# Kernel tuning notes

Measured on AMD Instinct MI355X. Metric: run time of the kernel, lower is better.

## Reference

```python
import jax, jax.numpy as jnp
import numpy as np

B, N, F, D = 8, 2048, 128, 128


def setup_inputs() -> dict:
    key = jax.random.key(0)
    k1, k2, k3 = jax.random.split(key, 3)
    inputs = jax.random.normal(k1, (B, N, F), dtype=jnp.float32)
    adj = jax.random.uniform(k2, (B, N, N), dtype=jnp.float32)  # nonneg weights -> positive degrees
    W_kernel = jax.random.normal(k3, (F, D), dtype=jnp.float32) * (1.0 / np.sqrt(F))
    W_bias = jnp.zeros((D,), dtype=jnp.float32)
    return {"inputs": inputs, "adj": adj, "W_kernel": W_kernel, "W_bias": W_bias}


def _normalize_adjacency(adj):
    # D^{-1/2} A D^{-1/2}: same math as diag-matmul chain, via broadcast scaling
    d = jnp.sum(adj, axis=-1)                      # [B, N]
    d_sqrt_inv = jnp.power(d, -0.5)
    d_sqrt_inv = jnp.where(jnp.isinf(d_sqrt_inv), 0.0, d_sqrt_inv)
    return d_sqrt_inv[..., :, None] * adj * d_sqrt_inv[..., None, :]


def reference(inputs, adj, W_kernel, W_bias):
    adj_norm = _normalize_adjacency(adj)           # [B, N, N]
    feats = inputs @ W_kernel + W_bias             # [B, N, D]
    out = jnp.einsum('bnm,bmd->bnd', adj_norm, feats)
    return jax.nn.relu(out)
```

## Files before the change

### kernel.cpp

```cpp
#include <hip/hip_runtime.h>
#include <hip/hip_bf16.h>
#include <stdint.h>

#define B_ 8
#define N_ 2048
#define F_ 128
#define D_ 128

typedef short bf16x8 __attribute__((ext_vector_type(8)));
typedef float f32x4 __attribute__((ext_vector_type(4)));

__device__ __forceinline__ unsigned short f2bf(float f) {
    unsigned u = __float_as_uint(f);
    u += 0x7fffu + ((u >> 16) & 1u);
    return (unsigned short)(u >> 16);
}

__global__ __launch_bounds__(256) void k_degwt(const float* __restrict__ adj,
                                               const float* __restrict__ W,
                                               float* __restrict__ rs,
                                               unsigned short* __restrict__ Wt) {
    if (blockIdx.x < 4096) {
        const int wave = threadIdx.x >> 6, lane = threadIdx.x & 63;
        const int row = blockIdx.x * 4 + wave;
        const float4* p = (const float4*)(adj + (size_t)row * N_);
        float s = 0.f;
#pragma unroll
        for (int j = 0; j < 8; ++j) {
            float4 v = p[j * 64 + lane];
            s += (v.x + v.y) + (v.z + v.w);
        }
#pragma unroll
        for (int m = 1; m < 64; m <<= 1) s += __shfl_xor(s, m, 64);
        if (lane == 0) rs[row] = (s > 0.f) ? (1.0f / sqrtf(s)) : 0.f;
    } else {
        int c = (blockIdx.x - 4096) * 256 + threadIdx.x;
        int d = c >> 4, f0 = (c & 15) * 8;
        union { bf16x8 v; unsigned short u[8]; } pk;
#pragma unroll
        for (int e = 0; e < 8; ++e) pk.u[e] = f2bf(W[(size_t)(f0 + e) * D_ + d]);
        *(bf16x8*)(Wt + (size_t)d * F_ + f0) = pk.v;
    }
}

__global__ __launch_bounds__(256) void k_feat(const float* __restrict__ x,
                                              const unsigned short* __restrict__ Wt,
                                              const float* __restrict__ bias,
                                              const float* __restrict__ rs,
                                              unsigned short* __restrict__ gt) {
    __shared__ __align__(16) unsigned char sX[64 * 128 * 2];
    __shared__ __align__(16) unsigned char sW[128 * 128 * 2];
    const int t = threadIdx.x;
    const int R0 = blockIdx.x * 64;

#pragma unroll
    for (int j = 0; j < 8; ++j) {
        int c = j * 256 + t;
        unsigned L = (unsigned)c * 16u;
        unsigned lg = L ^ (((L >> 8) & 7u) << 4);
        const unsigned char* src = (const unsigned char*)Wt + lg;
        __builtin_amdgcn_global_load_lds(
            (const __attribute__((address_space(1))) void*)src,
            (__attribute__((address_space(3))) void*)(sW + L), 16, 0, 0);
    }
#pragma unroll
    for (int j = 0; j < 4; ++j) {
        int c = j * 256 + t;
        int row = c >> 4, sub = c & 15;
        const float4* src = (const float4*)(x + (size_t)(R0 + row) * F_ + sub * 8);
        float4 v0 = src[0], v1 = src[1];
        union { bf16x8 v; unsigned short u[8]; } pk;
        pk.u[0] = f2bf(v0.x); pk.u[1] = f2bf(v0.y); pk.u[2] = f2bf(v0.z); pk.u[3] = f2bf(v0.w);
        pk.u[4] = f2bf(v1.x); pk.u[5] = f2bf(v1.y); pk.u[6] = f2bf(v1.z); pk.u[7] = f2bf(v1.w);
        unsigned byte = (unsigned)(row * 256 + sub * 16);
        byte ^= ((byte >> 8) & 7u) << 4;
        *(bf16x8*)(sX + byte) = pk.v;
    }
    __syncthreads();

    const int w = t >> 6, l = t & 63, lr = l & 15, lh = l >> 4;
    f32x4 acc[8];
#pragma unroll
    for (int j = 0; j < 8; ++j) acc[j] = (f32x4){0.f, 0.f, 0.f, 0.f};

#pragma unroll
    for (int ks = 0; ks < 4; ++ks) {
        unsigned abyte = (unsigned)((w * 16 + lr) * 256 + lh * 16 + ks * 64);
        abyte ^= ((abyte >> 8) & 7u) << 4;
        bf16x8 a = *(const bf16x8*)(sX + abyte);
#pragma unroll
        for (int j = 0; j < 8; ++j) {
            unsigned bbyte = (unsigned)((j * 16 + lr) * 256 + lh * 16 + ks * 64);
            bbyte ^= ((bbyte >> 8) & 7u) << 4;
            bf16x8 bb = *(const bf16x8*)(sW + bbyte);
            acc[j] = __builtin_amdgcn_mfma_f32_16x16x32_bf16(a, bb, acc[j], 0, 0, 0);
        }
    }

    const int m0 = R0 + w * 16 + lh * 4;
    float4 r4 = *(const float4*)(rs + m0);
    float rr[4] = {r4.x, r4.y, r4.z, r4.w};
#pragma unroll
    for (int j = 0; j < 8; ++j) {
        int d = j * 16 + lr;
        float bv = bias[d];
#pragma unroll
        for (int r = 0; r < 4; ++r) {
            int m = m0 + r;
            int b = m >> 11, n = m & (N_ - 1);
            gt[((size_t)b * D_ + d) * N_ + n] = f2bf((acc[j][r] + bv) * rr[r]);
        }
    }
}

__global__ __launch_bounds__(512) void k_gcn(const float* __restrict__ adj,
                                             const unsigned short* __restrict__ gt,
                                             const float* __restrict__ rs,
                                             float* __restrict__ out) {
    __shared__ __align__(16) unsigned char sA[2][32 * 128 * 2];
    __shared__ __align__(16) unsigned char sB[2][128 * 128 * 2];

    unsigned bid = blockIdx.x;
    unsigned wg = (bid & 7u) * 64u + (bid >> 3);
    const int b = (int)(wg >> 6);
    const int R0 = (int)(wg & 63u) * 32;

    const float* adjB = adj + (size_t)b * N_ * N_ + (size_t)R0 * N_;
    const unsigned short* gtB = gt + (size_t)b * D_ * N_;
    const float* rsB = rs + (size_t)b * N_;

    const int t = threadIdx.x;
    const int w = t >> 6, l = t & 63, lr = l & 15, lh = l >> 4;
    const int kg = w >> 2, cg = w & 3;

    const float* aSrc = adjB + (size_t)(t >> 4) * N_ + (t & 15) * 8;
    unsigned aL = (unsigned)((t >> 4) * 256 + (t & 15) * 16);
    aL ^= ((aL >> 8) & 7u) << 4;

    const unsigned short* bSrc[4];
    unsigned bL[4];
#pragma unroll
    for (int i = 0; i < 4; ++i) {
        unsigned c = (unsigned)(i * 512 + t);
        unsigned L = c * 16u;
        unsigned lg = L ^ (((L >> 8) & 7u) << 4);
        bL[i] = L;
        bSrc[i] = gtB + (size_t)(lg >> 8) * N_ + ((lg & 255u) >> 1);
    }

    auto issueB = [&](int buf, int k0) {
        unsigned char* pB = sB[buf];
#pragma unroll
        for (int i = 0; i < 4; ++i) {
            __builtin_amdgcn_global_load_lds(
                (const __attribute__((address_space(1))) void*)(bSrc[i] + k0),
                (__attribute__((address_space(3))) void*)(pB + bL[i]), 16, 0, 0);
        }
    };

    f32x4 acc[2][2];
#pragma unroll
    for (int i = 0; i < 2; ++i)
#pragma unroll
        for (int jn = 0; jn < 2; ++jn) acc[i][jn] = (f32x4){0.f, 0.f, 0.f, 0.f};

    issueB(0, 0);
    float4 a0 = *(const float4*)(aSrc);
    float4 a1 = *(const float4*)(aSrc + 4);

    const int NITER = N_ / 128;
    for (int it = 0; it < NITER; ++it) {
        const int cur = it & 1;
        float4 n0 = a0, n1 = a1;
        if (it + 1 < NITER) {
            issueB(cur ^ 1, (it + 1) * 128);
            const float* s = aSrc + (it + 1) * 128;
            n0 = *(const float4*)(s);
            n1 = *(const float4*)(s + 4);
            asm volatile("s_waitcnt vmcnt(6)" ::: "memory");
        } else {
            asm volatile("s_waitcnt vmcnt(0)" ::: "memory");
        }
        __builtin_amdgcn_sched_barrier(0);

        {
            unsigned u0, u1, u2, u3;
            asm("v_cvt_pk_bf16_f32 %0, %1, %2" : "=v"(u0) : "v"(a0.x), "v"(a0.y));
            asm("v_cvt_pk_bf16_f32 %0, %1, %2" : "=v"(u1) : "v"(a0.z), "v"(a0.w));
            asm("v_cvt_pk_bf16_f32 %0, %1, %2" : "=v"(u2) : "v"(a1.x), "v"(a1.y));
            asm("v_cvt_pk_bf16_f32 %0, %1, %2" : "=v"(u3) : "v"(a1.z), "v"(a1.w));
            union { unsigned u[4]; bf16x8 v; } pk;
            pk.u[0] = u0; pk.u[1] = u1; pk.u[2] = u2; pk.u[3] = u3;
            *(bf16x8*)(sA[cur] + aL) = pk.v;
        }
        asm volatile("s_waitcnt lgkmcnt(0)" ::: "memory");
        __builtin_amdgcn_sched_barrier(0);
        __builtin_amdgcn_s_barrier();

        const unsigned char* pA = sA[cur];
        const unsigned char* pB = sB[cur];
#pragma unroll
        for (int kk2 = 0; kk2 < 2; ++kk2) {
            const int kk = kg * 2 + kk2;
            bf16x8 a[2], bb[2];
#pragma unroll
            for (int i = 0; i < 2; ++i) {
                unsigned byte = (unsigned)((i * 16 + lr) * 256 + lh * 16 + kk * 64);
                byte ^= ((byte >> 8) & 7u) << 4;
                a[i] = *(const bf16x8*)(pA + byte);
            }
#pragma unroll
            for (int jn = 0; jn < 2; ++jn) {
                int d = cg * 32 + jn * 16 + lr;
                unsigned byte = (unsigned)(d * 256 + lh * 16 + kk * 64);
                byte ^= ((byte >> 8) & 7u) << 4;
                bb[jn] = *(const bf16x8*)(pB + byte);
            }
#pragma unroll
            for (int i = 0; i < 2; ++i)
#pragma unroll
                for (int jn = 0; jn < 2; ++jn)
                    acc[i][jn] = __builtin_amdgcn_mfma_f32_16x16x32_bf16(a[i], bb[jn], acc[i][jn], 0, 0, 0);
        }
        __builtin_amdgcn_s_barrier();

        a0 = n0; a1 = n1;
    }

    float* sO = (float*)sA;
    if (kg == 1) {
#pragma unroll
        for (int i = 0; i < 2; ++i)
#pragma unroll
            for (int jn = 0; jn < 2; ++jn)
#pragma unroll
                for (int r = 0; r < 4; ++r) {
                    int rowl = i * 16 + lh * 4 + r;
                    int d = cg * 32 + jn * 16 + lr;
                    sO[rowl * 128 + d] = acc[i][jn][r];
                }
    }
    __syncthreads();
    if (kg == 0) {
#pragma unroll
        for (int i = 0; i < 2; ++i) {
            float4 r4 = *(const float4*)(rsB + R0 + i * 16 + lh * 4);
            float rr[4] = {r4.x, r4.y, r4.z, r4.w};
#pragma unroll
            for (int r = 0; r < 4; ++r) {
                int rowl = i * 16 + lh * 4 + r;
#pragma unroll
                for (int jn = 0; jn < 2; ++jn) {
                    int d = cg * 32 + jn * 16 + lr;
                    float v = (acc[i][jn][r] + sO[rowl * 128 + d]) * rr[r];
                    out[((size_t)(b * N_ + R0 + rowl)) * D_ + d] = fmaxf(v, 0.f);
                }
            }
        }
    }
}

extern "C" void kernel_launch(void* const* d_in, const int* in_sizes, int n_in,
                              void* d_out, int out_size, void* d_ws, size_t ws_size,
                              hipStream_t stream) {
    const float* inputs = (const float*)d_in[0];
    const float* adj    = (const float*)d_in[1];
    const float* Wk     = (const float*)d_in[2];
    const float* Wb     = (const float*)d_in[3];
    float* out = (float*)d_out;

    float* rs = (float*)d_ws;
    unsigned short* gt = (unsigned short*)((char*)d_ws + 65536);
    unsigned short* Wt = (unsigned short*)((char*)d_ws + 65536 + (size_t)B_ * D_ * N_ * 2);

    k_degwt<<<4096 + 8, 256, 0, stream>>>(adj, Wk, rs, Wt);
    k_feat <<<(B_ * N_) / 64, 256, 0, stream>>>(inputs, Wk == nullptr ? nullptr : Wt, Wb, rs, gt);
    k_gcn  <<<B_ * (N_ / 32), 512, 0, stream>>>(adj, gt, rs, out);
}
```

Measured before the change: 55.40 us.

## Convert adjacency to bf16 during degree pass and stream it via LDS loads

The degree-sum kernel now also writes a bf16 copy of the adjacency matrix. The aggregation kernel then loads that copy directly into LDS with global_load_lds, instead of loading fp32 into registers and converting. This halves the bytes the main GEMM reads and removes the register conversion and LDS store from its loop. The cost is an extra 64 MiB write in the first kernel, so total traffic is roughly unchanged unless the bf16 copy is served from cache.

```diff
diff --git a/kernel.cpp b/kernel.cpp
--- a/kernel.cpp
+++ b/kernel.cpp
@@ -19,16 +19,23 @@
 __global__ __launch_bounds__(256) void k_degwt(const float* __restrict__ adj,
                                                const float* __restrict__ W,
                                                float* __restrict__ rs,
+                                               unsigned short* __restrict__ adjbf,
                                                unsigned short* __restrict__ Wt) {
     if (blockIdx.x < 4096) {
         const int wave = threadIdx.x >> 6, lane = threadIdx.x & 63;
         const int row = blockIdx.x * 4 + wave;
         const float4* p = (const float4*)(adj + (size_t)row * N_);
+        unsigned short* q = adjbf + (size_t)row * N_;
         float s = 0.f;
 #pragma unroll
         for (int j = 0; j < 8; ++j) {
             float4 v = p[j * 64 + lane];
             s += (v.x + v.y) + (v.z + v.w);
+            unsigned u0, u1;
+            asm("v_cvt_pk_bf16_f32 %0, %1, %2" : "=v"(u0) : "v"(v.x), "v"(v.y));
+            asm("v_cvt_pk_bf16_f32 %0, %1, %2" : "=v"(u1) : "v"(v.z), "v"(v.w));
+            uint2 pk; pk.x = u0; pk.y = u1;
+            *(uint2*)(q + j * 256 + lane * 4) = pk;
         }
 #pragma unroll
         for (int m = 1; m < 64; m <<= 1) s += __shfl_xor(s, m, 64);
@@ -113,19 +120,19 @@
     }
 }
 
-__global__ __launch_bounds__(512) void k_gcn(const float* __restrict__ adj,
+__global__ __launch_bounds__(512) void k_gcn(const unsigned short* __restrict__ adjbf,
                                              const unsigned short* __restrict__ gt,
                                              const float* __restrict__ rs,
                                              float* __restrict__ out) {
-    __shared__ __align__(16) unsigned char sA[2][32 * 128 * 2];
-    __shared__ __align__(16) unsigned char sB[2][128 * 128 * 2];
+    __shared__ __align__(16) unsigned char sA[2][32 * 256];
+    __shared__ __align__(16) unsigned char sB[2][128 * 256];
 
     unsigned bid = blockIdx.x;
     unsigned wg = (bid & 7u) * 64u + (bid >> 3);
     const int b = (int)(wg >> 6);
     const int R0 = (int)(wg & 63u) * 32;
 
-    const float* adjB = adj + (size_t)b * N_ * N_ + (size_t)R0 * N_;
+    const unsigned short* adjB = adjbf + (size_t)(b * N_ + R0) * N_;
     const unsigned short* gtB = gt + (size_t)b * D_ * N_;
     const float* rsB = rs + (size_t)b * N_;
 
@@ -133,9 +140,10 @@
     const int w = t >> 6, l = t & 63, lr = l & 15, lh = l >> 4;
     const int kg = w >> 2, cg = w & 3;
 
-    const float* aSrc = adjB + (size_t)(t >> 4) * N_ + (t & 15) * 8;
-    unsigned aL = (unsigned)((t >> 4) * 256 + (t & 15) * 16);
-    aL ^= ((aL >> 8) & 7u) << 4;
+    const unsigned aL = (unsigned)t * 16u;
+    const unsigned aRow = aL >> 8;
+    const unsigned aWi = (aL & 255u) ^ ((aRow & 7u) << 4);
+    const unsigned short* aSrcBase = adjB + (size_t)aRow * N_ + (aWi >> 1);
 
     const unsigned short* bSrc[4];
     unsigned bL[4];
@@ -148,7 +156,7 @@
         bSrc[i] = gtB + (size_t)(lg >> 8) * N_ + ((lg & 255u) >> 1);
     }
 
-    auto issueB = [&](int buf, int k0) {
+    auto stage = [&](int buf, int k0) {
         unsigned char* pB = sB[buf];
 #pragma unroll
         for (int i = 0; i < 4; ++i) {
@@ -156,6 +164,9 @@
                 (const __attribute__((address_space(1))) void*)(bSrc[i] + k0),
                 (__attribute__((address_space(3))) void*)(pB + bL[i]), 16, 0, 0);
         }
+        __builtin_amdgcn_global_load_lds(
+            (const __attribute__((address_space(1))) void*)(aSrcBase + k0),
+            (__attribute__((address_space(3))) void*)(sA[buf] + aL), 16, 0, 0);
     };
 
     f32x4 acc[2][2];
@@ -164,36 +175,17 @@
 #pragma unroll
         for (int jn = 0; jn < 2; ++jn) acc[i][jn] = (f32x4){0.f, 0.f, 0.f, 0.f};
 
-    issueB(0, 0);
-    float4 a0 = *(const float4*)(aSrc);
-    float4 a1 = *(const float4*)(aSrc + 4);
+    stage(0, 0);
 
     const int NITER = N_ / 128;
     for (int it = 0; it < NITER; ++it) {
         const int cur = it & 1;
-        float4 n0 = a0, n1 = a1;
         if (it + 1 < NITER) {
-            issueB(cur ^ 1, (it + 1) * 128);
-            const float* s = aSrc + (it + 1) * 128;
-            n0 = *(const float4*)(s);
-            n1 = *(const float4*)(s + 4);
-            asm volatile("s_waitcnt vmcnt(6)" ::: "memory");
+            stage(cur ^ 1, (it + 1) * 128);
+            asm volatile("s_waitcnt vmcnt(5)" ::: "memory");
         } else {
             asm volatile("s_waitcnt vmcnt(0)" ::: "memory");
         }
-        __builtin_amdgcn_sched_barrier(0);
-
-        {
-            unsigned u0, u1, u2, u3;
-            asm("v_cvt_pk_bf16_f32 %0, %1, %2" : "=v"(u0) : "v"(a0.x), "v"(a0.y));
-            asm("v_cvt_pk_bf16_f32 %0, %1, %2" : "=v"(u1) : "v"(a0.z), "v"(a0.w));
-            asm("v_cvt_pk_bf16_f32 %0, %1, %2" : "=v"(u2) : "v"(a1.x), "v"(a1.y));
-            asm("v_cvt_pk_bf16_f32 %0, %1, %2" : "=v"(u3) : "v"(a1.z), "v"(a1.w));
-            union { unsigned u[4]; bf16x8 v; } pk;
-            pk.u[0] = u0; pk.u[1] = u1; pk.u[2] = u2; pk.u[3] = u3;
-            *(bf16x8*)(sA[cur] + aL) = pk.v;
-        }
-        asm volatile("s_waitcnt lgkmcnt(0)" ::: "memory");
         __builtin_amdgcn_sched_barrier(0);
         __builtin_amdgcn_s_barrier();
 
@@ -205,15 +197,16 @@
             bf16x8 a[2], bb[2];
 #pragma unroll
             for (int i = 0; i < 2; ++i) {
-                unsigned byte = (unsigned)((i * 16 + lr) * 256 + lh * 16 + kk * 64);
-                byte ^= ((byte >> 8) & 7u) << 4;
+                unsigned row = (unsigned)(i * 16 + lr);
+                unsigned byte = row * 256 + (unsigned)(lh * 16 + kk * 64);
+                byte ^= (row & 7u) << 4;
                 a[i] = *(const bf16x8*)(pA + byte);
             }
 #pragma unroll
             for (int jn = 0; jn < 2; ++jn) {
-                int d = cg * 32 + jn * 16 + lr;
-                unsigned byte = (unsigned)(d * 256 + lh * 16 + kk * 64);
-                byte ^= ((byte >> 8) & 7u) << 4;
+                unsigned d = (unsigned)(cg * 32 + jn * 16 + lr);
+                unsigned byte = d * 256 + (unsigned)(lh * 16 + kk * 64);
+                byte ^= (d & 7u) << 4;
                 bb[jn] = *(const bf16x8*)(pB + byte);
             }
 #pragma unroll
@@ -223,8 +216,6 @@
                     acc[i][jn] = __builtin_amdgcn_mfma_f32_16x16x32_bf16(a[i], bb[jn], acc[i][jn], 0, 0, 0);
         }
         __builtin_amdgcn_s_barrier();
-
-        a0 = n0; a1 = n1;
     }
 
     float* sO = (float*)sA;
@@ -269,11 +260,13 @@
     const float* Wb     = (const float*)d_in[3];
     float* out = (float*)d_out;
 
-    float* rs = (float*)d_ws;
-    unsigned short* gt = (unsigned short*)((char*)d_ws + 65536);
-    unsigned short* Wt = (unsigned short*)((char*)d_ws + 65536 + (size_t)B_ * D_ * N_ * 2);
-
-    k_degwt<<<4096 + 8, 256, 0, stream>>>(adj, Wk, rs, Wt);
-    k_feat <<<(B_ * N_) / 64, 256, 0, stream>>>(inputs, Wk == nullptr ? nullptr : Wt, Wb, rs, gt);
-    k_gcn  <<<B_ * (N_ / 32), 512, 0, stream>>>(adj, gt, rs, out);
-}
+    char* ws = (char*)d_ws;
+    float* rs           = (float*)ws;
+    unsigned short* gt  = (unsigned short*)(ws + (1 << 20));
+    unsigned short* Wt  = (unsigned short*)(ws + (6 << 20));
+    unsigned short* adjbf = (unsigned short*)(ws + (8 << 20));
+
+    k_degwt<<<4096 + 8, 256, 0, stream>>>(adj, Wk, rs, adjbf, Wt);
+    k_feat <<<(B_ * N_) / 64, 256, 0, stream>>>(inputs, Wt, Wb, rs, gt);
+    k_gcn  <<<B_ * (N_ / 32), 512, 0, stream>>>(adjbf, gt, rs, out);
+}
```

Measured after the change: 58.23 us. +5.1%, slower.
